# Kernel tuning notes

Hardware: AMD Instinct MI355X
Metric: run time of the kernel (lower is better)

Reference implementation:

```python
import jax, jax.numpy as jnp
import numpy as np
import math

BLOCK = 8
N_COEFF = BLOCK * BLOCK  # 64
N_SAMPLE = 250
SEED = 0  # args.seed

# zigzag order: flat index m*8+n from the hardcoded loc table
ZIGZAG = jnp.array([
    0, 1, 8, 16, 9, 2, 3, 10, 17, 24, 32, 25, 18, 11, 4, 5,
    12, 19, 26, 33, 40, 48, 41, 34, 27, 20, 13, 6, 7, 14, 21, 28,
    35, 42, 49, 56, 57, 50, 43, 36, 29, 22, 15, 23, 30, 37, 44, 51,
    58, 59, 52, 45, 38, 31, 39, 46, 53, 60, 61, 54, 47, 55, 62, 63
], dtype=jnp.int32)


def dct_matrix():
    Q = np.zeros((BLOCK, BLOCK), dtype=np.float32)
    Q[0, :] = math.sqrt(1.0 / BLOCK)
    for i in range(1, BLOCK):
        for j in range(BLOCK):
            Q[i, j] = math.sqrt(2.0 / BLOCK) * math.cos((2 * j + 1) * math.pi * i / (2.0 * BLOCK))
    return jnp.asarray(Q)


def setup_inputs() -> dict:
    key = jax.random.key(0)
    x = jax.random.uniform(key, (64, 3, 512, 512), dtype=jnp.float32)
    return {"x": x}


def reference(x):
    Q = dct_matrix()
    # rgb -> ycbcr, luminance channel only (module discards Cb/Cr)
    x255 = x * 255.0
    y = (0.299 * x255[:, 0] + 0.587 * x255[:, 1] + 0.114 * x255[:, 2]) / 255.0  # [B,H,W]
    B, H, W = y.shape
    a, b = H // BLOCK, W // BLOCK
    # split into 8x8 blocks: [B, a, b, 8, 8]
    blocks = y.reshape(B, a, BLOCK, b, BLOCK).transpose(0, 1, 3, 2, 4)
    # per-block 2D DCT: Q @ block @ Q^T, batched as one einsum
    dct = jnp.einsum('ij,nabjk,lk->nabil', Q, blocks, Q)  # [B,a,b,8,8]
    image_dct_result = dct.transpose(0, 1, 3, 2, 4).reshape(B, 1, H, W)
    # zigzag gather over flattened block coefficients -> [B, 64, a*b]
    dist = dct.reshape(B, a * b, N_COEFF)[:, :, ZIGZAG].transpose(0, 2, 1)
    # per (sample, coefficient) random permutation sampling of 250 blocks
    keys = jax.random.split(jax.random.key(SEED), B * N_COEFF)
    idx = jax.vmap(lambda k: jax.random.permutation(k, a * b)[:N_SAMPLE])(keys)
    idx = idx.reshape(B, N_COEFF, N_SAMPLE)
    dct_coeff_sample = jnp.take_along_axis(dist, idx, axis=2)  # [B,64,250]
    return image_dct_result, dct_coeff_sample
```

## Files before the change

kernel.cpp:

```cpp
#include <hip/hip_runtime.h>
#include <hip/hip_bf16.h>
#include <cstdint>


#define BATCH 64
#define HW 512
#define NBLK 4096
#define NSAMPLE 250
#define IMG_ELEMS (HW * HW)

#define A0 0.35355339059327373f
#define A1 0.49039264020161522f
#define A2 0.46193976625564337f
#define A3 0.41573480615127262f
#define A4 0.35355339059327379f
#define A5 0.27778511650980111f
#define A6 0.19134171618254492f
#define A7 0.09754516100806412f

__constant__ float Qc[8][8] = {
    { A0,  A0,  A0,  A0,  A0,  A0,  A0,  A0},
    { A1,  A3,  A5,  A7, -A7, -A5, -A3, -A1},
    { A2,  A6, -A6, -A2, -A2, -A6,  A6,  A2},
    { A3, -A7, -A1, -A5,  A5,  A1,  A7, -A3},
    { A4, -A4, -A4,  A4,  A4, -A4, -A4,  A4},
    { A5, -A1,  A7,  A3, -A3, -A7,  A1, -A5},
    { A6, -A2,  A2, -A6, -A6,  A2, -A2,  A6},
    { A7, -A5,  A3, -A1,  A1, -A3,  A5, -A7},
};

__constant__ int ZIGZAG[64] = {
    0, 1, 8, 16, 9, 2, 3, 10, 17, 24, 32, 25, 18, 11, 4, 5,
    12, 19, 26, 33, 40, 48, 41, 34, 27, 20, 13, 6, 7, 14, 21, 28,
    35, 42, 49, 56, 57, 50, 43, 36, 29, 22, 15, 23, 30, 37, 44, 51,
    58, 59, 52, 45, 38, 31, 39, 46, 53, 60, 61, 54, 47, 55, 62, 63
};

__device__ __forceinline__ uint32_t rotl32(uint32_t v, int d) {
    return (v << d) | (v >> (32 - d));
}

__device__ __forceinline__ void tf2x32(uint32_t k0, uint32_t k1,
                                       uint32_t x0, uint32_t x1,
                                       uint32_t& o0, uint32_t& o1) {
    uint32_t ks0 = k0, ks1 = k1, ks2 = k0 ^ k1 ^ 0x1BD11BDAu;
    x0 += ks0; x1 += ks1;
#define TF_R(r) { x0 += x1; x1 = rotl32(x1, r); x1 ^= x0; }
    TF_R(13) TF_R(15) TF_R(26) TF_R(6)
    x0 += ks1; x1 += ks2 + 1u;
    TF_R(17) TF_R(29) TF_R(16) TF_R(24)
    x0 += ks2; x1 += ks0 + 2u;
    TF_R(13) TF_R(15) TF_R(26) TF_R(6)
    x0 += ks0; x1 += ks1 + 3u;
    TF_R(17) TF_R(29) TF_R(16) TF_R(24)
    x0 += ks1; x1 += ks2 + 4u;
    TF_R(13) TF_R(15) TF_R(26) TF_R(6)
    x0 += ks2; x1 += ks0 + 5u;
#undef TF_R
    o0 = x0; o1 = x1;
}

__device__ __forceinline__ void build4096(
    uint32_t s0, uint32_t s1,
    uint32_t* __restrict__ pack32, uint32_t* __restrict__ hist32,
    int tid, int w, int lane, uint32_t* __restrict__ wsum) {
    uint16_t* hist16 = (uint16_t*)hist32;

    __syncthreads();
#pragma unroll
    for (int q = 0; q < 4; ++q) hist32[tid + q * 512] = 0u;
    uint32_t keys[8];
#pragma unroll
    for (int e = 0; e < 8; ++e) {
        uint32_t o0, o1;
        tf2x32(s0, s1, 0u, (uint32_t)(tid + e * 512), o0, o1);
        keys[e] = o0 ^ o1;
    }
    __syncthreads();

    uint32_t ord[8];
#pragma unroll
    for (int e = 0; e < 8; ++e) {
        uint32_t bkt = keys[e] >> 20;
        uint32_t sh = (bkt & 1) << 4;
        uint32_t old = atomicAdd(&hist32[bkt >> 1], 1u << sh);
        ord[e] = (old >> sh) & 0xFFFFu;
    }
    __syncthreads();

    uint4 wv = ((const uint4*)hist32)[tid];
    uint32_t c0 = wv.x & 0xFFFFu, c1 = wv.x >> 16;
    uint32_t c2 = wv.y & 0xFFFFu, c3 = wv.y >> 16;
    uint32_t c4 = wv.z & 0xFFFFu, c5 = wv.z >> 16;
    uint32_t c6 = wv.w & 0xFFFFu, c7 = wv.w >> 16;
    uint32_t ssum = c0 + c1 + c2 + c3 + c4 + c5 + c6 + c7;
    uint32_t sc = ssum;
#pragma unroll
    for (int off = 1; off < 64; off <<= 1) {
        uint32_t t = __shfl_up(sc, off);
        if (lane >= off) sc += t;
    }
    if (lane == 63) wsum[w] = sc;
    __syncthreads();
    uint32_t ex = sc - ssum;
    for (int ww = 0; ww < w; ++ww) ex += wsum[ww];
    uint32_t p1 = ex + c0, p2 = p1 + c1, p3 = p2 + c2, p4 = p3 + c3;
    uint32_t p5 = p4 + c4, p6 = p5 + c5, p7 = p6 + c6, p8 = p7 + c7;
    uint4 ov;
    ov.x = p1 | (p2 << 16); ov.y = p3 | (p4 << 16);
    ov.z = p5 | (p6 << 16); ov.w = p7 | (p8 << 16);
    ((uint4*)hist32)[tid] = ov;
    __syncthreads();

#pragma unroll
    for (int e = 0; e < 8; ++e) {
        uint32_t bkt = keys[e] >> 20;
        uint32_t start = bkt ? (uint32_t)hist16[bkt - 1] : 0u;
        pack32[start + ord[e]] =
            ((keys[e] & 0xFFFFFu) << 12) | (uint32_t)(tid + e * 512);
    }
}

__device__ __forceinline__ uint32_t select4096(
    const uint16_t* __restrict__ hist16, const uint32_t* __restrict__ pack32,
    uint32_t s) {
    uint32_t lo = 0, hi = 4095;
#pragma unroll
    for (int it = 0; it < 12; ++it) {
        uint32_t mid = (lo + hi) >> 1;
        if ((uint32_t)hist16[mid] > s) hi = mid; else lo = mid + 1;
    }
    uint32_t b = lo;
    uint32_t start = b ? (uint32_t)hist16[b - 1] : 0u;
    uint32_t L = (uint32_t)hist16[b] - start;
    uint32_t c = pack32[start];
    if (L > 1) {
        uint32_t k = s - start;
        for (uint32_t cand = 0; cand < L; ++cand) {
            uint32_t cc = pack32[start + cand];
            uint32_t cnt = 0;
            for (uint32_t o = 0; o < L; ++o)
                cnt += (pack32[start + o] < cc) ? 1u : 0u;
            if (cnt == k) { c = cc; break; }
        }
    }
    return c & 0xFFFu;
}

__global__ __launch_bounds__(512) void fused_kernel(const float* __restrict__ x,
                                                    float* __restrict__ out,
                                                    uint32_t* __restrict__ ws) {
    __shared__ __align__(16) uint8_t smem[25088];
    __shared__ uint32_t wsum[8];

    const int tid = threadIdx.x;

    if (blockIdx.x & 1) {
        float* ylds = (float*)smem + (tid >> 8) * 2048;
        const int t = tid & 255;
        const int wg = ((int)blockIdx.x & ~1) | (tid >> 8);
        const int b = wg >> 7;
        const int ai = (wg >> 1) & 63;
        const int h = wg & 1;
        const int row0 = ai * 8;
        const int colbase = h * 256;

        {
            const int k = t >> 5;
            const int cg = t & 31;
            size_t off = (size_t)b * 3 * IMG_ELEMS + (size_t)(row0 + k) * HW +
                         colbase + cg * 8;
            float4 r0 = *(const float4*)(x + off);
            float4 r1 = *(const float4*)(x + off + 4);
            float4 g0 = *(const float4*)(x + off + IMG_ELEMS);
            float4 g1 = *(const float4*)(x + off + IMG_ELEMS + 4);
            float4 b0 = *(const float4*)(x + off + 2 * IMG_ELEMS);
            float4 b1 = *(const float4*)(x + off + 2 * IMG_ELEMS + 4);
            float R[8] = {r0.x, r0.y, r0.z, r0.w, r1.x, r1.y, r1.z, r1.w};
            float G[8] = {g0.x, g0.y, g0.z, g0.w, g1.x, g1.y, g1.z, g1.w};
            float B[8] = {b0.x, b0.y, b0.z, b0.w, b1.x, b1.y, b1.z, b1.w};
#pragma unroll
            for (int jj = 0; jj < 8; ++jj) {
                float y = (0.299f * (R[jj] * 255.0f) + 0.587f * (G[jj] * 255.0f) +
                           0.114f * (B[jj] * 255.0f)) / 255.0f;
                ylds[k * 256 + jj * 32 + cg] = y;
            }
        }
        __syncthreads();

        const int i = t >> 5;
        const int bi = t & 31;
        float qrow[8];
#pragma unroll
        for (int k = 0; k < 8; ++k) qrow[k] = Qc[i][k];

        float acc[8];
#pragma unroll
        for (int j = 0; j < 8; ++j) acc[j] = 0.0f;
#pragma unroll
        for (int k = 0; k < 8; ++k) {
#pragma unroll
            for (int j = 0; j < 8; ++j)
                acc[j] += qrow[k] * ylds[k * 256 + j * 32 + bi];
        }

        float d[8];
#pragma unroll
        for (int j = 0; j < 8; ++j) {
            float s = 0.0f;
#pragma unroll
            for (int k = 0; k < 8; ++k) s += acc[k] * Qc[j][k];
            d[j] = s;
        }
        float4* o = (float4*)(out + (size_t)b * IMG_ELEMS +
                              (size_t)(row0 + i) * HW + colbase + bi * 8);
        o[0] = make_float4(d[0], d[1], d[2], d[3]);
        o[1] = make_float4(d[4], d[5], d[6], d[7]);
    } else {
        uint32_t* pack32 = (uint32_t*)smem;
        uint32_t* hist32 = (uint32_t*)(smem + 16384);
        uint16_t* jsel = (uint16_t*)(smem + 24576);
        uint16_t* hist16 = (uint16_t*)hist32;

        const int w = tid >> 6;
        const int lane = tid & 63;
        const int gb = (int)blockIdx.x >> 1;

        uint32_t k0, k1, n0, n1, sA0, sA1, sB0, sB1;
        tf2x32(0u, 0u, 0u, (uint32_t)gb, k0, k1);
        tf2x32(k0, k1, 0u, 0u, n0, n1);
        tf2x32(k0, k1, 0u, 1u, sA0, sA1);
        tf2x32(n0, n1, 0u, 1u, sB0, sB1);

        build4096(sB0, sB1, pack32, hist32, tid, w, lane, wsum);
        __syncthreads();
        if (tid < NSAMPLE)
            jsel[tid] = (uint16_t)select4096(hist16, pack32, (uint32_t)tid);

        build4096(sA0, sA1, pack32, hist32, tid, w, lane, wsum);
        __syncthreads();

        int b = gb >> 6, c = gb & 63;
        int z = ZIGZAG[c];
        int i0z = z >> 3, j0z = z & 7;
        if (tid < NSAMPLE) {
            uint32_t i = select4096(hist16, pack32, (uint32_t)jsel[tid]);
            int ai = (int)i >> 6, bi = (int)i & 63;
            ws[(size_t)gb * 256 + tid] =
                (uint32_t)((size_t)b * IMG_ELEMS +
                           (size_t)(ai * 8 + i0z) * HW + (bi * 8 + j0z));
        }
    }
}

__global__ __launch_bounds__(256) void gather_kernel(
    const float* __restrict__ img, const uint32_t* __restrict__ ws,
    float* __restrict__ out2) {
    const int gb = blockIdx.x;
    const int s = threadIdx.x;
    if (s < NSAMPLE)
        out2[(size_t)gb * NSAMPLE + s] = img[ws[(size_t)gb * 256 + s]];
}

extern "C" void kernel_launch(void* const* d_in, const int* in_sizes, int n_in,
                              void* d_out, int out_size, void* d_ws, size_t ws_size,
                              hipStream_t stream) {
    const float* x = (const float*)d_in[0];
    float* out = (float*)d_out;
    uint32_t* ws = (uint32_t*)d_ws;
    fused_kernel<<<BATCH * 128, 512, 0, stream>>>(x, out, ws);
    gather_kernel<<<BATCH * 64, 256, 0, stream>>>(
        out, ws, out + (size_t)BATCH * IMG_ELEMS);
}
```

Before: 422.4 us.

## Compute one 8x8 DCT block per thread and rebalance DCT/sampling block mix

```diff
diff --git a/kernel.cpp b/kernel.cpp
--- a/kernel.cpp
+++ b/kernel.cpp
@@ -147,75 +147,86 @@
     return c & 0xFFFu;
 }
 
-__global__ __launch_bounds__(512) void fused_kernel(const float* __restrict__ x,
-                                                    float* __restrict__ out,
-                                                    uint32_t* __restrict__ ws) {
+__global__ __launch_bounds__(512, 8) void fused_kernel(
+    const float* __restrict__ x, float* __restrict__ out,
+    uint32_t* __restrict__ ws) {
     __shared__ __align__(16) uint8_t smem[25088];
     __shared__ uint32_t wsum[8];
 
     const int tid = threadIdx.x;
-
-    if (blockIdx.x & 1) {
-        float* ylds = (float*)smem + (tid >> 8) * 2048;
-        const int t = tid & 255;
-        const int wg = ((int)blockIdx.x & ~1) | (tid >> 8);
-        const int b = wg >> 7;
-        const int ai = (wg >> 1) & 63;
-        const int h = wg & 1;
-        const int row0 = ai * 8;
-        const int colbase = h * 256;
-
-        {
-            const int k = t >> 5;
-            const int cg = t & 31;
-            size_t off = (size_t)b * 3 * IMG_ELEMS + (size_t)(row0 + k) * HW +
-                         colbase + cg * 8;
-            float4 r0 = *(const float4*)(x + off);
-            float4 r1 = *(const float4*)(x + off + 4);
-            float4 g0 = *(const float4*)(x + off + IMG_ELEMS);
-            float4 g1 = *(const float4*)(x + off + IMG_ELEMS + 4);
-            float4 b0 = *(const float4*)(x + off + 2 * IMG_ELEMS);
-            float4 b1 = *(const float4*)(x + off + 2 * IMG_ELEMS + 4);
-            float R[8] = {r0.x, r0.y, r0.z, r0.w, r1.x, r1.y, r1.z, r1.w};
-            float G[8] = {g0.x, g0.y, g0.z, g0.w, g1.x, g1.y, g1.z, g1.w};
-            float B[8] = {b0.x, b0.y, b0.z, b0.w, b1.x, b1.y, b1.z, b1.w};
-#pragma unroll
-            for (int jj = 0; jj < 8; ++jj) {
-                float y = (0.299f * (R[jj] * 255.0f) + 0.587f * (G[jj] * 255.0f) +
-                           0.114f * (B[jj] * 255.0f)) / 255.0f;
-                ylds[k * 256 + jj * 32 + cg] = y;
+    const int grp = (int)blockIdx.x / 9;
+    const int rem = (int)blockIdx.x % 9;
+
+    if (rem == 8) {
+        int g = grp * 512 + tid;
+        int b = g >> 12;
+        int rr = g & 4095;
+        int ai = rr >> 6, bi = rr & 63;
+        int row0 = ai * 8, col0 = bi * 8;
+        size_t ib = (size_t)b * 3 * IMG_ELEMS;
+        size_t ob = (size_t)b * IMG_ELEMS;
+
+        for (int half = 0; half < 2; ++half) {
+            float acc[4][8];
+#pragma unroll
+            for (int i2 = 0; i2 < 4; ++i2)
+#pragma unroll
+                for (int j = 0; j < 8; ++j) acc[i2][j] = 0.0f;
+
+#pragma unroll 1
+            for (int k = 0; k < 8; ++k) {
+                size_t off = ib + (size_t)(row0 + k) * HW + col0;
+                float y[8];
+                {
+                    float4 r0 = *(const float4*)(x + off);
+                    float4 g0 = *(const float4*)(x + off + IMG_ELEMS);
+                    float4 b0 = *(const float4*)(x + off + 2 * IMG_ELEMS);
+                    y[0] = (0.299f * (r0.x * 255.0f) + 0.587f * (g0.x * 255.0f) +
+                            0.114f * (b0.x * 255.0f)) / 255.0f;
+                    y[1] = (0.299f * (r0.y * 255.0f) + 0.587f * (g0.y * 255.0f) +
+                            0.114f * (b0.y * 255.0f)) / 255.0f;
+                    y[2] = (0.299f * (r0.z * 255.0f) + 0.587f * (g0.z * 255.0f) +
+                            0.114f * (b0.z * 255.0f)) / 255.0f;
+                    y[3] = (0.299f * (r0.w * 255.0f) + 0.587f * (g0.w * 255.0f) +
+                            0.114f * (b0.w * 255.0f)) / 255.0f;
+                }
+                {
+                    float4 r1 = *(const float4*)(x + off + 4);
+                    float4 g1 = *(const float4*)(x + off + IMG_ELEMS + 4);
+                    float4 b1 = *(const float4*)(x + off + 2 * IMG_ELEMS + 4);
+                    y[4] = (0.299f * (r1.x * 255.0f) + 0.587f * (g1.x * 255.0f) +
+                            0.114f * (b1.x * 255.0f)) / 255.0f;
+                    y[5] = (0.299f * (r1.y * 255.0f) + 0.587f * (g1.y * 255.0f) +
+                            0.114f * (b1.y * 255.0f)) / 255.0f;
+                    y[6] = (0.299f * (r1.z * 255.0f) + 0.587f * (g1.z * 255.0f) +
+                            0.114f * (b1.z * 255.0f)) / 255.0f;
+                    y[7] = (0.299f * (r1.w * 255.0f) + 0.587f * (g1.w * 255.0f) +
+                            0.114f * (b1.w * 255.0f)) / 255.0f;
+                }
+#pragma unroll
+                for (int i2 = 0; i2 < 4; ++i2) {
+                    float q = Qc[half * 4 + i2][k];
+#pragma unroll
+                    for (int j = 0; j < 8; ++j) acc[i2][j] += q * y[j];
+                }
+            }
+
+#pragma unroll
+            for (int i2 = 0; i2 < 4; ++i2) {
+                float d[8];
+#pragma unroll
+                for (int j = 0; j < 8; ++j) {
+                    float s = 0.0f;
+#pragma unroll
+                    for (int k = 0; k < 8; ++k) s += acc[i2][k] * Qc[j][k];
+                    d[j] = s;
+                }
+                float4* o = (float4*)(out + ob +
+                                      (size_t)(row0 + half * 4 + i2) * HW + col0);
+                o[0] = make_float4(d[0], d[1], d[2], d[3]);
+                o[1] = make_float4(d[4], d[5], d[6], d[7]);
             }
         }
-        __syncthreads();
-
-        const int i = t >> 5;
-        const int bi = t & 31;
-        float qrow[8];
-#pragma unroll
-        for (int k = 0; k < 8; ++k) qrow[k] = Qc[i][k];
-
-        float acc[8];
-#pragma unroll
-        for (int j = 0; j < 8; ++j) acc[j] = 0.0f;
-#pragma unroll
-        for (int k = 0; k < 8; ++k) {
-#pragma unroll
-            for (int j = 0; j < 8; ++j)
-                acc[j] += qrow[k] * ylds[k * 256 + j * 32 + bi];
-        }
-
-        float d[8];
-#pragma unroll
-        for (int j = 0; j < 8; ++j) {
-            float s = 0.0f;
-#pragma unroll
-            for (int k = 0; k < 8; ++k) s += acc[k] * Qc[j][k];
-            d[j] = s;
-        }
-        float4* o = (float4*)(out + (size_t)b * IMG_ELEMS +
-                              (size_t)(row0 + i) * HW + colbase + bi * 8);
-        o[0] = make_float4(d[0], d[1], d[2], d[3]);
-        o[1] = make_float4(d[4], d[5], d[6], d[7]);
     } else {
         uint32_t* pack32 = (uint32_t*)smem;
         uint32_t* hist32 = (uint32_t*)(smem + 16384);
@@ -224,7 +235,7 @@
 
         const int w = tid >> 6;
         const int lane = tid & 63;
-        const int gb = (int)blockIdx.x >> 1;
+        const int gb = grp * 8 + rem;
 
         uint32_t k0, k1, n0, n1, sA0, sA1, sB0, sB1;
         tf2x32(0u, 0u, 0u, (uint32_t)gb, k0, k1);
@@ -268,7 +279,7 @@
     const float* x = (const float*)d_in[0];
     float* out = (float*)d_out;
     uint32_t* ws = (uint32_t*)d_ws;
-    fused_kernel<<<BATCH * 128, 512, 0, stream>>>(x, out, ws);
+    fused_kernel<<<512 * 9, 512, 0, stream>>>(x, out, ws);
     gather_kernel<<<BATCH * 64, 256, 0, stream>>>(
         out, ws, out + (size_t)BATCH * IMG_ELEMS);
 }
```

New measurement: 387.3 us. 1.09x faster.
